# Kernel tuning notes

Hardware: AMD Instinct MI355X
Metric: run time of the kernel (lower is better)

Reference implementation:

```python
import jax, jax.numpy as jnp
import numpy as np

HEADS = 16
DIM_HEAD = 64
SCALE = DIM_HEAD ** -0.5


def shift(x):
    # Transformer-XL relative shift trick. x: [..., i, j] -> [..., i, j]
    *pre, i, j = x.shape
    x = jnp.concatenate([x, jnp.zeros((*pre, i, i), x.dtype)], axis=-1)
    l = i + j - 1
    x = x.reshape(*pre, -1)
    pad = (-x.shape[-1]) % l
    x = jnp.concatenate([x, jnp.zeros((*pre, pad), x.dtype)], axis=-1)
    x = x.reshape(*pre, -1, l)
    return x[..., :i, i - 1:]


def setup_inputs() -> dict:
    key = jax.random.key(0)
    ks = jax.random.split(key, 8)
    b, t, e = 2, 1024, 1024
    mem_len, lmem_len = 1024, 128
    kv_len = t + mem_len + lmem_len
    return {
        "x": jax.random.normal(ks[0], (b, t, e), jnp.float32),
        "mem": jax.random.normal(ks[1], (b, mem_len, e), jnp.float32),
        "lmem": jax.random.normal(ks[2], (b, lmem_len, e), jnp.float32),
        "pos_emb": jax.random.normal(ks[3], (HEADS, kv_len, DIM_HEAD), jnp.float32),
        "input_mask": jnp.ones((b, t), bool),
        "Wq": jax.random.normal(ks[4], (e, e), jnp.float32) * 0.02,
        "Wkv": jax.random.normal(ks[5], (e, 2 * e), jnp.float32) * 0.02,
        "Wout": jax.random.normal(ks[6], (e, e), jnp.float32) * 0.02,
        "bout": jnp.zeros((e,), jnp.float32),
    }


def reference(x, mem, lmem, pos_emb, input_mask, Wq, Wkv, Wout, bout):
    b, t, e = x.shape
    h, dh = HEADS, DIM_HEAD
    mem_len, lmem_len = mem.shape[1], lmem.shape[1]
    total_mem = mem_len + lmem_len

    q = x @ Wq
    kv_input = jnp.concatenate([lmem, mem, x], axis=1)  # [b, kv_len, e]
    kv_len = kv_input.shape[1]
    k, v = jnp.split(kv_input @ Wkv, 2, axis=-1)

    def merge_heads(z):
        return z.reshape(b, -1, h, dh).transpose(0, 2, 1, 3)  # [b, h, n, dh]

    q, k, v = merge_heads(q), merge_heads(k), merge_heads(v)

    dots = jnp.einsum('bhid,bhjd->bhij', q, k) * SCALE  # [b, h, t, kv_len]

    pe = pos_emb[:, -kv_len:].astype(q.dtype)
    pos_dots = jnp.einsum('bhid,hjd->bhij', q, pe) * SCALE
    dots = dots + shift(pos_dots)

    mask_value = -jnp.finfo(dots.dtype).max

    pad_mask = input_mask[:, None, :, None] & input_mask[:, None, None, :]
    pad_mask = jnp.pad(pad_mask, ((0, 0), (0, 0), (0, 0), (total_mem, 0)), constant_values=True)
    dots = jnp.where(pad_mask, dots, mask_value)

    causal = jnp.triu(jnp.ones((t, t + total_mem), bool), k=1 + total_mem)
    dots = jnp.where(causal[None, None], mask_value, dots)

    attn = jax.nn.softmax(dots, axis=-1)
    out = jnp.einsum('bhij,bhjd->bhid', attn, v)
    out = out.transpose(0, 2, 1, 3).reshape(b, t, -1)
    return out @ Wout + bout
```

## Files before the change

### kernel.cpp

```cpp
#include <hip/hip_runtime.h>


typedef unsigned int   u32;
typedef unsigned short u16;
typedef unsigned long long u64;
typedef __attribute__((ext_vector_type(8))) short short8;
typedef __attribute__((ext_vector_type(4))) float f32x4;
typedef __attribute__((ext_vector_type(4))) u32   u32x4;

#define DEVI static __device__ __forceinline__
#define MFMA_BF16 __builtin_amdgcn_mfma_f32_16x16x32_bf16

DEVI u16 f2bf(float f) {
  u32 u = __builtin_bit_cast(u32, f);
  return (u16)((u + 0x7FFFu + ((u >> 16) & 1u)) >> 16);
}
DEVI float bf2f(u16 h) { u32 u = (u32)h << 16; return __builtin_bit_cast(float, u); }
DEVI u32 pk2(float lo, float hi) { return (u32)f2bf(lo) | ((u32)f2bf(hi) << 16); }
DEVI u32 cvtpk(float lo, float hi) {
  u32 r;
  asm("v_cvt_pk_bf16_f32 %0, %1, %2" : "=v"(r) : "v"(lo), "v"(hi));
  return r;
}

constexpr int T_ = 1024, E_ = 1024, KV = 2176, H_ = 16;
constexpr float QSCALE = 0.125f * 1.44269504088896f;

__global__ void k_prep_kvin(const float* __restrict__ x, const float* __restrict__ mem,
                            const float* __restrict__ lmem, u16* __restrict__ kvin) {
  int u = blockIdx.x * 256 + threadIdx.x;
  int b = u / (KV * E_ / 8);
  int r = u % (KV * E_ / 8);
  int j = r >> 7;
  int e8 = (r & 127) << 3;
  const float* src;
  if (j < 128)        src = lmem + ((size_t)(b * 128 + j) * E_ + e8);
  else if (j < 1152)  src = mem  + ((size_t)(b * 1024 + (j - 128)) * E_ + e8);
  else                src = x    + ((size_t)(b * 1024 + (j - 1152)) * E_ + e8);
  float4 a = ((const float4*)src)[0];
  float4 c = ((const float4*)src)[1];
  u32x4 o = { pk2(a.x, a.y), pk2(a.z, a.w), pk2(c.x, c.y), pk2(c.z, c.w) };
  *(u32x4*)(kvin + (size_t)u * 8) = o;
}

__global__ void k_prep_pe(const float* __restrict__ pos, u16* __restrict__ pe) {
  size_t u = (size_t)blockIdx.x * 256 + threadIdx.x;
  float4 a = ((const float4*)(pos + u * 8))[0];
  float4 c = ((const float4*)(pos + u * 8))[1];
  u32x4 o = { pk2(a.x, a.y), pk2(a.z, a.w), pk2(c.x, c.y), pk2(c.z, c.w) };
  *(u32x4*)(pe + u * 8) = o;
}

__global__ void k_transp(const float* __restrict__ src, u16* __restrict__ dst, int K, int N) {
  __shared__ float tile[32][33];
  int n0 = blockIdx.x * 32, k0 = blockIdx.y * 32;
  int tx = threadIdx.x, ty = threadIdx.y;
#pragma unroll
  for (int s = 0; s < 4; s++) tile[ty + 8 * s][tx] = src[(size_t)(k0 + ty + 8 * s) * N + n0 + tx];
  __syncthreads();
#pragma unroll
  for (int s = 0; s < 4; s++)
    dst[(size_t)(n0 + ty + 8 * s) * K + k0 + tx] = f2bf(tile[tx][ty + 8 * s]);
}

__global__ __launch_bounds__(256, 2)
void k_gemm_qkv(const u16* __restrict__ kvin, const u16* __restrict__ WallT,
                u16* __restrict__ qb, u16* __restrict__ kb, u16* __restrict__ vtb) {
  int bid = blockIdx.x;
  int b = bid / 336;
  int r = bid % 336;
  int nt, mt;
  if (r < 64) { nt = r >> 3; mt = 9 + (r & 7); }
  else { r -= 64; nt = 8 + r / 17; mt = r % 17; }

  const u16* A  = kvin + ((size_t)b * KV + (size_t)mt * 128) * E_;
  const u16* Bm = WallT + (size_t)nt * 128 * E_;

  __shared__ u16 As[2][128 * 40];
  __shared__ u16 Bs[2][128 * 40];

  int t = threadIdx.x;
  int wid = t >> 6, lane = t & 63;
  int wr = wid >> 1, wc = wid & 1;
  int l15 = lane & 15, l4 = lane >> 4;

  f32x4 acc[4][4] = {};
  int arow = t >> 2, aslot = t & 3;

  u32x4 ra[2], rb[2];
  auto ld = [&](int kt_) {
    int k0 = kt_ * 32;
#pragma unroll
    for (int p = 0; p < 2; p++) {
      ra[p] = *(const u32x4*)(A  + (size_t)(arow + 64 * p) * E_ + k0 + aslot * 8);
      rb[p] = *(const u32x4*)(Bm + (size_t)(arow + 64 * p) * E_ + k0 + aslot * 8);
    }
  };
  auto st = [&](int buf) {
#pragma unroll
    for (int p = 0; p < 2; p++) {
      *(u32x4*)(As[buf] + (arow + 64 * p) * 40 + aslot * 8) = ra[p];
      *(u32x4*)(Bs[buf] + (arow + 64 * p) * 40 + aslot * 8) = rb[p];
    }
  };

  ld(0); st(0); ld(1);
  for (int kt = 0; kt < 32; kt++) {
    __syncthreads();
    int buf = kt & 1;
    short8 af[4], bfv[4];
#pragma unroll
    for (int m = 0; m < 4; m++)
      af[m] = *(const short8*)(As[buf] + (wr * 64 + m * 16 + l15) * 40 + l4 * 8);
#pragma unroll
    for (int n = 0; n < 4; n++)
      bfv[n] = *(const short8*)(Bs[buf] + (wc * 64 + n * 16 + l15) * 40 + l4 * 8);
#pragma unroll
    for (int m = 0; m < 4; m++)
#pragma unroll
      for (int n = 0; n < 4; n++)
        acc[m][n] = MFMA_BF16(af[m], bfv[n], acc[m][n], 0, 0, 0);
    if (kt + 1 < 32) st(buf ^ 1);
    if (kt + 2 < 32) ld(kt + 2);
  }
  int grow_base = mt * 128 + wr * 64;
  int ncol_base = nt * 128 + wc * 64;
  if (nt < 8) {
#pragma unroll
    for (int m = 0; m < 4; m++)
#pragma unroll
      for (int n = 0; n < 4; n++) {
        int col = ncol_base + n * 16 + l15;
        int head = col >> 6, d = col & 63;
#pragma unroll
        for (int rg = 0; rg < 4; rg++) {
          int row = grow_base + m * 16 + l4 * 4 + rg - 1152;
          qb[(((size_t)b * 16 + head) * 1024 + row) * 64 + d] = f2bf(acc[m][n][rg] * QSCALE);
        }
      }
  } else if (nt < 16) {
#pragma unroll
    for (int m = 0; m < 4; m++)
#pragma unroll
      for (int n = 0; n < 4; n++) {
        int c = ncol_base + n * 16 + l15 - 1024;
        int head = c >> 6, d = c & 63;
#pragma unroll
        for (int rg = 0; rg < 4; rg++) {
          int row = grow_base + m * 16 + l4 * 4 + rg;
          kb[(((size_t)b * 16 + head) * KV + row) * 64 + d] = f2bf(acc[m][n][rg]);
        }
      }
  } else {
#pragma unroll
    for (int m = 0; m < 4; m++)
#pragma unroll
      for (int n = 0; n < 4; n++) {
        int c = ncol_base + n * 16 + l15 - 2048;
        int head = c >> 6, d = c & 63;
        int jb = grow_base + m * 16 + l4 * 4;
        u64 pv = (u64)f2bf(acc[m][n][0]) | ((u64)f2bf(acc[m][n][1]) << 16)
               | ((u64)f2bf(acc[m][n][2]) << 32) | ((u64)f2bf(acc[m][n][3]) << 48);
        *(u64*)(vtb + (((size_t)b * 16 + head) * 64 + d) * KV + jb) = pv;
      }
  }
}

__global__ __launch_bounds__(256, 2)
void k_attn(const u16* __restrict__ qb, const u16* __restrict__ kb,
            const u16* __restrict__ vtb, const u16* __restrict__ peb,
            u16* __restrict__ ao) {
  int bid = blockIdx.x;
  int xcd = bid & 7;
  int itr = (bid >> 3) & 15;
  int g   = bid >> 7;
  int it  = (g >= 2) ? (15 - itr) : itr;
  int bh = g * 8 + xcd;
  int b = bh >> 4, h = bh & 15;
  int i0 = it * 64;

  __shared__ u16 Klds[2][64][72];
  __shared__ u16 Vt[2][64][72];
  __shared__ u16 Band[64][136];
  __shared__ u16 Pb[4][16][72];

  int t = threadIdx.x, wid = t >> 6, lane = t & 63;
  int l15 = lane & 15, l4 = lane >> 4;
  int il = wid * 16 + l15;
  int srow = t >> 3, ssl = t & 7;

  const u16* kbase  = kb  + (size_t)bh * KV * 64;
  const u16* vtbase = vtb + (size_t)bh * 64 * KV;
  const u16* pebase = peb + (size_t)h * KV * 64;

  const u16* qptr = qb + ((size_t)bh * 1024 + i0 + il) * 64 + l4 * 8;
  short8 qf0 = *(const short8*)qptr;
  short8 qf1 = *(const short8*)(qptr + 32);

  f32x4 Of[4] = {};
  float mr = -1e30f, lr = 0.f;
  int njt = it + 19;

  u32x4 rk0, rk1, rv0, rv1;
  auto load_regs = [&](int jt_) {
    int j0_ = jt_ * 64;
    rk0 = *(const u32x4*)(kbase + (size_t)(j0_ + srow) * 64 + ssl * 8);
    rk1 = *(const u32x4*)(kbase + (size_t)(j0_ + srow + 32) * 64 + ssl * 8);
    rv0 = *(const u32x4*)(vtbase + (size_t)srow * KV + j0_ + ssl * 8);
    rv1 = *(const u32x4*)(vtbase + (size_t)(srow + 32) * KV + j0_ + ssl * 8);
  };
  auto store_tile = [&](int buf) {
    *(u32x4*)(&Klds[buf][srow][ssl * 8]) = rk0;
    *(u32x4*)(&Klds[buf][srow + 32][ssl * 8]) = rk1;
    *(u32x4*)(&Vt[buf][srow][ssl * 8]) = rv0;
    *(u32x4*)(&Vt[buf][srow + 32][ssl * 8]) = rv1;
  };
  auto load_pe = [&](int prb, short8* pf) {
#pragma unroll
    for (int rc = 0; rc < 4; rc++) {
      int rr = prb + rc * 16 + l15; rr = rr > 2175 ? 2175 : rr;
#pragma unroll
      for (int kk = 0; kk < 2; kk++)
        pf[rc * 2 + kk] = *(const short8*)(pebase + (size_t)rr * 64 + kk * 32 + l4 * 8);
    }
  };
  auto band_mfma_store = [&](int prb, const short8* pf) {
    f32x4 acc[4];
    __builtin_amdgcn_s_setprio(1);
#pragma unroll
    for (int rc = 0; rc < 4; rc++) {
      f32x4 a = {};
      a = MFMA_BF16(pf[rc * 2 + 0], qf0, a, 0, 0, 0);
      a = MFMA_BF16(pf[rc * 2 + 1], qf1, a, 0, 0, 0);
      acc[rc] = a;
    }
    __builtin_amdgcn_s_setprio(0);
#pragma unroll
    for (int rc = 0; rc < 4; rc++) {
      int rb = prb + rc * 16 + l4 * 4 + il + 1;
      u32 w01 = cvtpk(acc[rc][0], acc[rc][1]);
      u32 w23 = cvtpk(acc[rc][2], acc[rc][3]);
      Band[il][rb & 127]       = (u16)w01;
      Band[il][(rb + 1) & 127] = (u16)(w01 >> 16);
      Band[il][(rb + 2) & 127] = (u16)w23;
      Band[il][(rb + 3) & 127] = (u16)(w23 >> 16);
    }
  };

  load_regs(0);
  store_tile(0);
  short8 pf[8];
  load_pe(960 - i0, pf);
  band_mfma_store(960 - i0, pf);
  load_pe(1024 - i0, pf);
  load_regs(1);

  int cur = 0;
  for (int jt = 0; jt < njt; jt++) {
    bool domask = (jt == njt - 1);
    __syncthreads();

    f32x4 sc[4];
    __builtin_amdgcn_s_setprio(1);
#pragma unroll
    for (int jc = 0; jc < 4; jc++) {
      f32x4 a = {};
      short8 k0 = *(const short8*)(&Klds[cur][jc * 16 + l15][l4 * 8]);
      short8 k1 = *(const short8*)(&Klds[cur][jc * 16 + l15][32 + l4 * 8]);
      a = MFMA_BF16(k0, qf0, a, 0, 0, 0);
      a = MFMA_BF16(k1, qf1, a, 0, 0, 0);
      sc[jc] = a;
    }
    __builtin_amdgcn_s_setprio(0);

    band_mfma_store(1024 + 64 * jt - i0, pf);
    if (jt + 1 < njt) load_pe(1024 + 64 * (jt + 1) - i0, pf);

    short8 vf[8];
#pragma unroll
    for (int df = 0; df < 4; df++)
#pragma unroll
      for (int kk = 0; kk < 2; kk++)
        vf[df * 2 + kk] = *(const short8*)(&Vt[cur][df * 16 + l15][kk * 32 + l4 * 8]);

    asm volatile("s_waitcnt lgkmcnt(0)" ::: "memory");
    __builtin_amdgcn_sched_barrier(0);

    float P[4][4];
    float mx = -1e30f;
    int cb0 = ((jt - it) & 1) << 6;
#pragma unroll
    for (int jc = 0; jc < 4; jc++) {
      u64 bl = *(const u64*)(&Band[il][cb0 + jc * 16 + l4 * 4]);
#pragma unroll
      for (int rg = 0; rg < 4; rg++) {
        int jj = jc * 16 + l4 * 4 + rg;
        float v = sc[jc][rg] + bf2f((u16)(bl >> (16 * rg)));
        if (domask && (jj > il)) v = -1e30f;
        P[jc][rg] = v;
        mx = fmaxf(mx, v);
      }
    }
    mx = fmaxf(mx, __shfl_xor(mx, 16, 64));
    mx = fmaxf(mx, __shfl_xor(mx, 32, 64));
    if (!__all(mx <= mr + 8.0f)) {
      float mnew = fmaxf(mr, mx);
      float fac = exp2f(mr - mnew);
      mr = mnew;
      lr *= fac;
#pragma unroll
      for (int dc = 0; dc < 4; dc++) Of[dc] *= fac;
    }
    float ps = 0.f;
#pragma unroll
    for (int jc = 0; jc < 4; jc++)
#pragma unroll
      for (int rg = 0; rg < 4; rg++) {
        float p = exp2f(P[jc][rg] - mr);
        P[jc][rg] = p;
        ps += p;
      }
    ps += __shfl_xor(ps, 16, 64);
    ps += __shfl_xor(ps, 32, 64);
    lr += ps;

#pragma unroll
    for (int jc = 0; jc < 4; jc++) {
      int cb = jc * 16 + l4 * 4;
      *(u32*)(&Pb[wid][l15][cb])     = cvtpk(P[jc][0], P[jc][1]);
      *(u32*)(&Pb[wid][l15][cb + 2]) = cvtpk(P[jc][2], P[jc][3]);
    }
    asm volatile("s_waitcnt lgkmcnt(0)" ::: "memory");
    __builtin_amdgcn_sched_barrier(0);

    short8 pB0 = *(const short8*)(&Pb[wid][l15][l4 * 8]);
    short8 pB1 = *(const short8*)(&Pb[wid][l15][32 + l4 * 8]);
    __builtin_amdgcn_s_setprio(1);
#pragma unroll
    for (int df = 0; df < 4; df++) {
      Of[df] = MFMA_BF16(vf[df * 2 + 0], pB0, Of[df], 0, 0, 0);
      Of[df] = MFMA_BF16(vf[df * 2 + 1], pB1, Of[df], 0, 0, 0);
    }
    __builtin_amdgcn_s_setprio(0);

    if (jt + 1 < njt) {
      store_tile(cur ^ 1);
      if (jt + 2 < njt) load_regs(jt + 2);
    }
    cur ^= 1;
  }

  float inv = 1.0f / lr;
  size_t ob = ((size_t)b * 1024 + i0 + il) * 1024 + h * 64;
#pragma unroll
  for (int df = 0; df < 4; df++) {
    u64 pv = (u64)f2bf(Of[df][0] * inv)         | ((u64)f2bf(Of[df][1] * inv) << 16)
           | ((u64)f2bf(Of[df][2] * inv) << 32) | ((u64)f2bf(Of[df][3] * inv) << 48);
    *(u64*)(ao + ob + df * 16 + l4 * 4) = pv;
  }
}

__global__ __launch_bounds__(256, 2)
void k_gemm_out(const u16* __restrict__ ao, const u16* __restrict__ WoT,
                const float* __restrict__ bias, float* __restrict__ out) {
  int mt = blockIdx.x & 31, nt = blockIdx.x >> 5;
  const u16* A  = ao  + (size_t)mt * 64 * E_;
  const u16* Bm = WoT + (size_t)nt * 128 * E_;
  __shared__ u16 As[64 * 40];
  __shared__ u16 Bs[128 * 40];
  int t = threadIdx.x, wid = t >> 6, lane = t & 63;
  int wr = wid >> 1, wc = wid & 1, l15 = lane & 15, l4 = lane >> 4;
  f32x4 acc[2][4] = {};
  int arow = t >> 2, aslot = t & 3;

  u32x4 ra, rb[2];
  ra = *(const u32x4*)(A + (size_t)arow * E_ + aslot * 8);
#pragma unroll
  for (int p = 0; p < 2; p++)
    rb[p] = *(const u32x4*)(Bm + (size_t)(arow + 64 * p) * E_ + aslot * 8);
  for (int kt = 0; kt < 32; kt++) {
    __syncthreads();
    *(u32x4*)(As + arow * 40 + aslot * 8) = ra;
#pragma unroll
    for (int p = 0; p < 2; p++)
      *(u32x4*)(Bs + (arow + 64 * p) * 40 + aslot * 8) = rb[p];
    __syncthreads();
    if (kt + 1 < 32) {
      int k0 = (kt + 1) * 32;
      ra = *(const u32x4*)(A + (size_t)arow * E_ + k0 + aslot * 8);
#pragma unroll
      for (int p = 0; p < 2; p++)
        rb[p] = *(const u32x4*)(Bm + (size_t)(arow + 64 * p) * E_ + k0 + aslot * 8);
    }
    short8 af[2], bfv[4];
#pragma unroll
    for (int m = 0; m < 2; m++)
      af[m] = *(const short8*)(As + (wr * 32 + m * 16 + l15) * 40 + l4 * 8);
#pragma unroll
    for (int n = 0; n < 4; n++)
      bfv[n] = *(const short8*)(Bs + (wc * 64 + n * 16 + l15) * 40 + l4 * 8);
#pragma unroll
    for (int m = 0; m < 2; m++)
#pragma unroll
      for (int n = 0; n < 4; n++)
        acc[m][n] = MFMA_BF16(af[m], bfv[n], acc[m][n], 0, 0, 0);
  }
#pragma unroll
  for (int n = 0; n < 4; n++) {
    int col = nt * 128 + wc * 64 + n * 16 + l15;
    float bv = bias[col];
#pragma unroll
    for (int m = 0; m < 2; m++) {
      int row = mt * 64 + wr * 32 + m * 16 + l4 * 4;
#pragma unroll
      for (int rg = 0; rg < 4; rg++)
        out[(size_t)(row + rg) * E_ + col] = acc[m][n][rg] + bv;
    }
  }
}

extern "C" void kernel_launch(void* const* d_in, const int* in_sizes, int n_in,
                              void* d_out, int out_size, void* d_ws, size_t ws_size,
                              hipStream_t stream) {
  (void)in_sizes; (void)n_in; (void)out_size; (void)ws_size;
  const float* x    = (const float*)d_in[0];
  const float* mem  = (const float*)d_in[1];
  const float* lmem = (const float*)d_in[2];
  const float* pos  = (const float*)d_in[3];
  const float* Wq   = (const float*)d_in[5];
  const float* Wkv  = (const float*)d_in[6];
  const float* Wout = (const float*)d_in[7];
  const float* bout = (const float*)d_in[8];
  float* out = (float*)d_out;

  u16* kvin  = (u16*)d_ws;
  u16* pe    = kvin  + (size_t)2 * KV * E_;
  u16* WallT = pe    + (size_t)H_ * KV * 64;
  u16* WoT   = WallT + (size_t)3072 * E_;
  u16* qb    = WoT   + (size_t)E_ * E_;
  u16* kb    = qb    + (size_t)2 * H_ * T_ * 64;
  u16* vtb   = kb    + (size_t)2 * H_ * KV * 64;
  u16* ao    = vtb   + (size_t)2 * H_ * KV * 64;

  k_prep_kvin<<<2176, 256, 0, stream>>>(x, mem, lmem, kvin);
  k_prep_pe<<<1088, 256, 0, stream>>>(pos, pe);
  k_transp<<<dim3(32, 32), dim3(32, 8), 0, stream>>>(Wq,   WallT,             1024, 1024);
  k_transp<<<dim3(64, 32), dim3(32, 8), 0, stream>>>(Wkv,  WallT + 1024*1024, 1024, 2048);
  k_transp<<<dim3(32, 32), dim3(32, 8), 0, stream>>>(Wout, WoT,               1024, 1024);
  k_gemm_qkv<<<672, 256, 0, stream>>>(kvin, WallT, qb, kb, vtb);
  k_attn<<<512, 256, 0, stream>>>(qb, kb, vtb, pe, ao);
  k_gemm_out<<<256, 256, 0, stream>>>(ao, WoT, bout, out);
}
```

Before: 146.6 us.

## Merge prep kernels, drop attention diagonal masking branch, double-buffer output GEMM

Five preprocessing launches (activation cast, positional cast, three weight transposes) become one kernel that dispatches on block index, cutting launch overhead and tail gaps. In attention, the last diagonal tile now writes -inf into the positional band instead of computing it, which removes the per-element causal compare, and the next-tile PE prefetch is skipped for that final tile. The output GEMM gets double-buffered LDS with one barrier per k-step instead of two. The band trick relies on the shift layout putting exactly the masked entries in the ninf range, and removing the clamp on the PE row index assumes indices never pass the end.

```diff
diff --git a/kernel.cpp b/kernel.cpp
--- a/kernel.cpp
+++ b/kernel.cpp
@@ -26,35 +26,43 @@
 constexpr int T_ = 1024, E_ = 1024, KV = 2176, H_ = 16;
 constexpr float QSCALE = 0.125f * 1.44269504088896f;
 
-__global__ void k_prep_kvin(const float* __restrict__ x, const float* __restrict__ mem,
-                            const float* __restrict__ lmem, u16* __restrict__ kvin) {
-  int u = blockIdx.x * 256 + threadIdx.x;
-  int b = u / (KV * E_ / 8);
-  int r = u % (KV * E_ / 8);
-  int j = r >> 7;
-  int e8 = (r & 127) << 3;
-  const float* src;
-  if (j < 128)        src = lmem + ((size_t)(b * 128 + j) * E_ + e8);
-  else if (j < 1152)  src = mem  + ((size_t)(b * 1024 + (j - 128)) * E_ + e8);
-  else                src = x    + ((size_t)(b * 1024 + (j - 1152)) * E_ + e8);
-  float4 a = ((const float4*)src)[0];
-  float4 c = ((const float4*)src)[1];
-  u32x4 o = { pk2(a.x, a.y), pk2(a.z, a.w), pk2(c.x, c.y), pk2(c.z, c.w) };
-  *(u32x4*)(kvin + (size_t)u * 8) = o;
-}
-
-__global__ void k_prep_pe(const float* __restrict__ pos, u16* __restrict__ pe) {
-  size_t u = (size_t)blockIdx.x * 256 + threadIdx.x;
-  float4 a = ((const float4*)(pos + u * 8))[0];
-  float4 c = ((const float4*)(pos + u * 8))[1];
-  u32x4 o = { pk2(a.x, a.y), pk2(a.z, a.w), pk2(c.x, c.y), pk2(c.z, c.w) };
-  *(u32x4*)(pe + u * 8) = o;
-}
-
-__global__ void k_transp(const float* __restrict__ src, u16* __restrict__ dst, int K, int N) {
+__global__ void k_prep_all(const float* __restrict__ x, const float* __restrict__ mem,
+                           const float* __restrict__ lmem, const float* __restrict__ pos,
+                           const float* __restrict__ Wq, const float* __restrict__ Wkv,
+                           const float* __restrict__ Wout,
+                           u16* __restrict__ kvin, u16* __restrict__ pe,
+                           u16* __restrict__ WallT, u16* __restrict__ WoT) {
   __shared__ float tile[32][33];
-  int n0 = blockIdx.x * 32, k0 = blockIdx.y * 32;
-  int tx = threadIdx.x, ty = threadIdx.y;
+  int bid = blockIdx.x, t = threadIdx.x;
+  if (bid < 3264) {
+    if (bid < 2176) {
+      int u = bid * 256 + t;
+      int b = u / (KV * E_ / 8);
+      int r = u % (KV * E_ / 8);
+      int j = r >> 7;
+      int e8 = (r & 127) << 3;
+      const float* src;
+      if (j < 128)        src = lmem + ((size_t)(b * 128 + j) * E_ + e8);
+      else if (j < 1152)  src = mem  + ((size_t)(b * 1024 + (j - 128)) * E_ + e8);
+      else                src = x    + ((size_t)(b * 1024 + (j - 1152)) * E_ + e8);
+      float4 a = ((const float4*)src)[0];
+      float4 c = ((const float4*)src)[1];
+      u32x4 o = { pk2(a.x, a.y), pk2(a.z, a.w), pk2(c.x, c.y), pk2(c.z, c.w) };
+      *(u32x4*)(kvin + (size_t)u * 8) = o;
+    } else {
+      size_t u = (size_t)(bid - 2176) * 256 + t;
+      float4 a = ((const float4*)(pos + u * 8))[0];
+      float4 c = ((const float4*)(pos + u * 8))[1];
+      u32x4 o = { pk2(a.x, a.y), pk2(a.z, a.w), pk2(c.x, c.y), pk2(c.z, c.w) };
+      *(u32x4*)(pe + u * 8) = o;
+    }
+    return;
+  }
+  const float* src; u16* dst; int K, N, n0, k0;
+  if (bid < 4288)      { int r = bid - 3264; src = Wq;   dst = WallT;             K = 1024; N = 1024; n0 = (r & 31) * 32; k0 = (r >> 5) * 32; }
+  else if (bid < 6336) { int r = bid - 4288; src = Wkv;  dst = WallT + 1024*1024; K = 1024; N = 2048; n0 = (r & 63) * 32; k0 = (r >> 6) * 32; }
+  else                 { int r = bid - 6336; src = Wout; dst = WoT;               K = 1024; N = 1024; n0 = (r & 31) * 32; k0 = (r >> 5) * 32; }
+  int tx = t & 31, ty = t >> 5;
 #pragma unroll
   for (int s = 0; s < 4; s++) tile[ty + 8 * s][tx] = src[(size_t)(k0 + ty + 8 * s) * N + n0 + tx];
   __syncthreads();
@@ -218,7 +226,7 @@
   auto load_pe = [&](int prb, short8* pf) {
 #pragma unroll
     for (int rc = 0; rc < 4; rc++) {
-      int rr = prb + rc * 16 + l15; rr = rr > 2175 ? 2175 : rr;
+      int rr = prb + rc * 16 + l15;
 #pragma unroll
       for (int kk = 0; kk < 2; kk++)
         pf[rc * 2 + kk] = *(const short8*)(pebase + (size_t)rr * 64 + kk * 32 + l4 * 8);
@@ -246,6 +254,15 @@
       Band[il][(rb + 3) & 127] = (u16)(w23 >> 16);
     }
   };
+  auto band_ninf = [&](int prb) {
+#pragma unroll
+    for (int rc = 0; rc < 4; rc++) {
+      int rb = prb + rc * 16 + l4 * 4 + il + 1;
+#pragma unroll
+      for (int rg = 0; rg < 4; rg++)
+        Band[il][(rb + rg) & 127] = 0xFF80u;
+    }
+  };
 
   load_regs(0);
   store_tile(0);
@@ -257,7 +274,6 @@
 
   int cur = 0;
   for (int jt = 0; jt < njt; jt++) {
-    bool domask = (jt == njt - 1);
     __syncthreads();
 
     f32x4 sc[4];
@@ -273,8 +289,9 @@
     }
     __builtin_amdgcn_s_setprio(0);
 
-    band_mfma_store(1024 + 64 * jt - i0, pf);
-    if (jt + 1 < njt) load_pe(1024 + 64 * (jt + 1) - i0, pf);
+    if (jt == njt - 1) band_ninf(1024 + 64 * jt - i0);
+    else               band_mfma_store(1024 + 64 * jt - i0, pf);
+    if (jt + 2 < njt) load_pe(1024 + 64 * (jt + 1) - i0, pf);
 
     short8 vf[8];
 #pragma unroll
@@ -294,9 +311,7 @@
       u64 bl = *(const u64*)(&Band[il][cb0 + jc * 16 + l4 * 4]);
 #pragma unroll
       for (int rg = 0; rg < 4; rg++) {
-        int jj = jc * 16 + l4 * 4 + rg;
         float v = sc[jc][rg] + bf2f((u16)(bl >> (16 * rg)));
-        if (domask && (jj > il)) v = -1e30f;
         P[jc][rg] = v;
         mx = fmaxf(mx, v);
       }
@@ -366,44 +381,46 @@
   int mt = blockIdx.x & 31, nt = blockIdx.x >> 5;
   const u16* A  = ao  + (size_t)mt * 64 * E_;
   const u16* Bm = WoT + (size_t)nt * 128 * E_;
-  __shared__ u16 As[64 * 40];
-  __shared__ u16 Bs[128 * 40];
+  __shared__ u16 As[2][64 * 40];
+  __shared__ u16 Bs[2][128 * 40];
   int t = threadIdx.x, wid = t >> 6, lane = t & 63;
   int wr = wid >> 1, wc = wid & 1, l15 = lane & 15, l4 = lane >> 4;
   f32x4 acc[2][4] = {};
   int arow = t >> 2, aslot = t & 3;
 
   u32x4 ra, rb[2];
-  ra = *(const u32x4*)(A + (size_t)arow * E_ + aslot * 8);
-#pragma unroll
-  for (int p = 0; p < 2; p++)
-    rb[p] = *(const u32x4*)(Bm + (size_t)(arow + 64 * p) * E_ + aslot * 8);
+  auto ld = [&](int kt_) {
+    int k0 = kt_ * 32;
+    ra = *(const u32x4*)(A + (size_t)arow * E_ + k0 + aslot * 8);
+#pragma unroll
+    for (int p = 0; p < 2; p++)
+      rb[p] = *(const u32x4*)(Bm + (size_t)(arow + 64 * p) * E_ + k0 + aslot * 8);
+  };
+  auto st = [&](int buf) {
+    *(u32x4*)(As[buf] + arow * 40 + aslot * 8) = ra;
+#pragma unroll
+    for (int p = 0; p < 2; p++)
+      *(u32x4*)(Bs[buf] + (arow + 64 * p) * 40 + aslot * 8) = rb[p];
+  };
+
+  ld(0); st(0); ld(1);
   for (int kt = 0; kt < 32; kt++) {
     __syncthreads();
-    *(u32x4*)(As + arow * 40 + aslot * 8) = ra;
-#pragma unroll
-    for (int p = 0; p < 2; p++)
-      *(u32x4*)(Bs + (arow + 64 * p) * 40 + aslot * 8) = rb[p];
-    __syncthreads();
-    if (kt + 1 < 32) {
-      int k0 = (kt + 1) * 32;
-      ra = *(const u32x4*)(A + (size_t)arow * E_ + k0 + aslot * 8);
-#pragma unroll
-      for (int p = 0; p < 2; p++)
-        rb[p] = *(const u32x4*)(Bm + (size_t)(arow + 64 * p) * E_ + k0 + aslot * 8);
-    }
+    int buf = kt & 1;
     short8 af[2], bfv[4];
 #pragma unroll
     for (int m = 0; m < 2; m++)
-      af[m] = *(const short8*)(As + (wr * 32 + m * 16 + l15) * 40 + l4 * 8);
+      af[m] = *(const short8*)(As[buf] + (wr * 32 + m * 16 + l15) * 40 + l4 * 8);
 #pragma unroll
     for (int n = 0; n < 4; n++)
-      bfv[n] = *(const short8*)(Bs + (wc * 64 + n * 16 + l15) * 40 + l4 * 8);
+      bfv[n] = *(const short8*)(Bs[buf] + (wc * 64 + n * 16 + l15) * 40 + l4 * 8);
 #pragma unroll
     for (int m = 0; m < 2; m++)
 #pragma unroll
       for (int n = 0; n < 4; n++)
         acc[m][n] = MFMA_BF16(af[m], bfv[n], acc[m][n], 0, 0, 0);
+    if (kt + 1 < 32) st(buf ^ 1);
+    if (kt + 2 < 32) ld(kt + 2);
   }
 #pragma unroll
   for (int n = 0; n < 4; n++) {
@@ -442,11 +459,8 @@
   u16* vtb   = kb    + (size_t)2 * H_ * KV * 64;
   u16* ao    = vtb   + (size_t)2 * H_ * KV * 64;
 
-  k_prep_kvin<<<2176, 256, 0, stream>>>(x, mem, lmem, kvin);
-  k_prep_pe<<<1088, 256, 0, stream>>>(pos, pe);
-  k_transp<<<dim3(32, 32), dim3(32, 8), 0, stream>>>(Wq,   WallT,             1024, 1024);
-  k_transp<<<dim3(64, 32), dim3(32, 8), 0, stream>>>(Wkv,  WallT + 1024*1024, 1024, 2048);
-  k_transp<<<dim3(32, 32), dim3(32, 8), 0, stream>>>(Wout, WoT,               1024, 1024);
+  k_prep_all<<<7360, 256, 0, stream>>>(x, mem, lmem, pos, Wq, Wkv, Wout,
+                                       kvin, pe, WallT, WoT);
   k_gemm_qkv<<<672, 256, 0, stream>>>(kvin, WallT, qb, kb, vtb);
   k_attn<<<512, 256, 0, stream>>>(qb, kb, vtb, pe, ao);
   k_gemm_out<<<256, 256, 0, stream>>>(ao, WoT, bout, out);
```

After: 134.5 us. 8.2% less time.
